# Kernel optimization log

Measured on AMD Instinct MI355X. Metric: run time of the kernel, lower is better.

The kernel has to match this reference:

```python
import jax, jax.numpy as jnp
import numpy as np

N_EL = 16
N_NUC = 4
N_FEATS = 32
CUTOFF = 10.0
ION_POT = 0.5
ALPHA = 1.0
BATCH = 32768
HIDDEN = 64
I_IDX, J_IDX = np.triu_indices(N_EL, 1)  # electron pairs i<j
N_PAIRS = N_EL * N_NUC + N_EL * (N_EL - 1) // 2
D_IN = N_PAIRS * N_FEATS


def ssp(x):
    # shifted softplus: softplus(x) - log(2), so ssp(0) = 0
    return jax.nn.softplus(x) - jnp.log(2.0).astype(x.dtype)


def setup_inputs() -> dict:
    key = jax.random.key(0)
    ks = jax.random.split(key, 9)
    rs = jax.random.normal(ks[0], (BATCH, N_EL, 3), jnp.float32) * 2.0
    coords = jax.random.normal(ks[1], (N_NUC, 3), jnp.float32)
    charges = jnp.arange(1, N_NUC + 1, dtype=jnp.float32)
    W1 = jax.random.normal(ks[2], (D_IN, HIDDEN), jnp.float32) / jnp.sqrt(D_IN)
    b1 = jnp.zeros((HIDDEN,), jnp.float32)
    W2 = jax.random.normal(ks[3], (HIDDEN, HIDDEN), jnp.float32) / jnp.sqrt(HIDDEN)
    b2 = jnp.zeros((HIDDEN,), jnp.float32)
    W3 = jax.random.normal(ks[4], (HIDDEN, 1), jnp.float32) / jnp.sqrt(HIDDEN)
    b3 = jnp.zeros((1,), jnp.float32)
    return {"rs": rs, "coords": coords, "charges": charges,
            "W1": W1, "b1": b1, "W2": W2, "b2": b2, "W3": W3, "b3": b3}


def reference(rs, coords, charges, W1, b1, W2, b2, W3, b3):
    B = rs.shape[0]
    # electron-nucleus distances: [B, n_el, n_nuc]
    diff_nuc = rs[:, :, None, :] - coords[None, None, :, :]
    dists_nuc = jnp.sqrt(jnp.sum(diff_nuc * diff_nuc, axis=-1))
    # electron-electron distances for pairs i<j: [B, n_el*(n_el-1)//2]
    diff_el = rs[:, I_IDX, :] - rs[:, J_IDX, :]
    dists_el = jnp.sqrt(jnp.sum(diff_el * diff_el, axis=-1))
    dists = jnp.concatenate([dists_nuc.reshape(B, -1), dists_el], axis=1)  # [B, N_PAIRS]
    # Gaussian distance basis expansion
    qs = jnp.linspace(0.0, 1.0, N_FEATS, dtype=rs.dtype)
    mus = CUTOFF * qs ** 2
    sigmas = (1.0 + CUTOFF * qs) / 7.0
    xs = jnp.exp(-((dists[..., None] - mus) ** 2) / sigmas ** 2)  # [B, N_PAIRS, N_FEATS]
    xs = xs.reshape(B, -1)
    # small MLP with shifted-softplus activations
    h = ssp(xs @ W1 + b1)
    h = ssp(h @ W2 + b2)
    ys = (h @ W3 + b3)[:, 0]
    # nuclear asymptotic factor
    decay = jnp.sqrt(2.0 * ION_POT)
    terms = (charges[None, None, :] * dists_nuc + decay * ALPHA * dists_nuc ** 2) / (1.0 + ALPHA * dists_nuc)
    asymp = jnp.exp(-jnp.sum(terms, axis=(1, 2)))
    return jnp.exp(ys) * asymp
```

## Files before the change

### kernel.cpp

```cpp
#include <hip/hip_runtime.h>
#include <math.h>

#define N_EL    16
#define N_NUC   4
#define N_FEATS 32
#define N_PAIRS 184
#define HIDDEN  64
#define TB      32
#define BLOCK   256
#define DLD     185
#define H1LD    68
#define TPW     23
#define WS_PART_OFF (1 << 19)

typedef int   intx8    __attribute__((ext_vector_type(8)));
typedef float floatx16 __attribute__((ext_vector_type(16)));

__constant__ unsigned char c_I[120] = {
    0,0,0,0,0,0,0,0,0,0,0,0,0,0,0,
    1,1,1,1,1,1,1,1,1,1,1,1,1,1,
    2,2,2,2,2,2,2,2,2,2,2,2,2,
    3,3,3,3,3,3,3,3,3,3,3,3,
    4,4,4,4,4,4,4,4,4,4,4,
    5,5,5,5,5,5,5,5,5,5,
    6,6,6,6,6,6,6,6,6,
    7,7,7,7,7,7,7,7,
    8,8,8,8,8,8,8,
    9,9,9,9,9,9,
    10,10,10,10,10,
    11,11,11,11,
    12,12,12,
    13,13,
    14
};
__constant__ unsigned char c_J[120] = {
    1,2,3,4,5,6,7,8,9,10,11,12,13,14,15,
    2,3,4,5,6,7,8,9,10,11,12,13,14,15,
    3,4,5,6,7,8,9,10,11,12,13,14,15,
    4,5,6,7,8,9,10,11,12,13,14,15,
    5,6,7,8,9,10,11,12,13,14,15,
    6,7,8,9,10,11,12,13,14,15,
    7,8,9,10,11,12,13,14,15,
    8,9,10,11,12,13,14,15,
    9,10,11,12,13,14,15,
    10,11,12,13,14,15,
    11,12,13,14,15,
    12,13,14,15,
    13,14,15,
    14,15,
    15
};

__device__ __forceinline__ float ssp(float x) {
    float a = fabsf(x);
    return fmaxf(x, 0.0f) + log1pf(__expf(-a)) - 0.69314718056f;
}
__device__ __forceinline__ float redg(float v) {
    v += __shfl_xor(v, 1);
    v += __shfl_xor(v, 2);
    v += __shfl_xor(v, 4);
    return v;
}

__global__ __launch_bounds__(256)
void prep_w1_kernel(const float* __restrict__ W1, intx8* __restrict__ ws)
{
    __shared__ float w[2 * N_FEATS * HIDDEN];
    const int t = blockIdx.x;
    const float* src = W1 + (size_t)(2 * t) * (N_FEATS * HIDDEN);
    for (int k = threadIdx.x; k < 2 * N_FEATS * HIDDEN; k += 256) w[k] = src[k];
    __syncthreads();

    const int tid = threadIdx.x;
    if (tid >= 128) return;
    const int lane = tid & 63;
    const int nh   = tid >> 6;
    const int lh   = lane >> 5;
    const int col  = nh * 32 + (lane & 31);
    const int fb   = lh * 16;
    intx8 frag;
#pragma unroll
    for (int r = 0; r < 8; ++r) {
        const int pair = r >> 2;
        const int fo   = fb + ((r & 3) << 2);
        const float v0 = 64.0f * w[(pair * N_FEATS + fo + 0) * 64 + col];
        const float v1 = 64.0f * w[(pair * N_FEATS + fo + 1) * 64 + col];
        const float v2 = 64.0f * w[(pair * N_FEATS + fo + 2) * 64 + col];
        const float v3 = 64.0f * w[(pair * N_FEATS + fo + 3) * 64 + col];
        int d = __builtin_amdgcn_cvt_pk_fp8_f32(v0, v1, 0, false);
        d     = __builtin_amdgcn_cvt_pk_fp8_f32(v2, v3, d, true);
        frag[r] = d;
    }
    ws[(size_t)(t * 2 + nh) * 64 + lane] = frag;
}

__global__ __launch_bounds__(BLOCK)
void wfnet_gemm(const float* __restrict__ rs,
                const float* __restrict__ coords,
                const intx8* __restrict__ ws,
                float* __restrict__ partials)
{
    __shared__ float lds_rs[TB * N_EL * 3];
    __shared__ float lds_dist[TB * DLD];

    const int tid  = threadIdx.x;
    const int wave = tid >> 6;
    const int lane = tid & 63;
    const int m    = lane & 31;
    const int lh   = lane >> 5;

    {
        const float* rs_blk = rs + (size_t)blockIdx.x * (TB * N_EL * 3);
        for (int k = tid; k < TB * N_EL * 3; k += BLOCK) lds_rs[k] = rs_blk[k];
    }
    __syncthreads();

    {
        const int bl = tid >> 3, g = tid & 7;
        const float* myrs = lds_rs + bl * (N_EL * 3);
        float* dst = lds_dist + bl * DLD;
        for (int i = 0; i < 8; ++i) {
            const int p = g + 8 * i;
            const int e = p >> 2, n = p & 3;
            const float dx = myrs[e * 3 + 0] - coords[n * 3 + 0];
            const float dy = myrs[e * 3 + 1] - coords[n * 3 + 1];
            const float dz = myrs[e * 3 + 2] - coords[n * 3 + 2];
            dst[p] = sqrtf(dx * dx + dy * dy + dz * dz);
        }
        for (int i = 0; i < 15; ++i) {
            const int q  = g + 8 * i;
            const int ei = 3 * (int)c_I[q], ej = 3 * (int)c_J[q];
            const float dx = myrs[ei + 0] - myrs[ej + 0];
            const float dy = myrs[ei + 1] - myrs[ej + 1];
            const float dz = myrs[ei + 2] - myrs[ej + 2];
            dst[64 + q] = sqrtf(dx * dx + dy * dy + dz * dz);
        }
    }
    __syncthreads();

    const int f0 = lh * 16;
#define MKC(P, FF) float P##1, P##0; { \
    const float fq = (float)(FF) * (1.0f / 31.0f); \
    const float mu = 10.0f * fq * fq; \
    const float is = 7.0f / (1.0f + 10.0f * fq); \
    P##1 = is * 3.3972871404442143f; \
    P##0 = -mu * P##1; }
    MKC(F0_,  f0 + 0)  MKC(F1_,  f0 + 1)  MKC(F2_,  f0 + 2)  MKC(F3_,  f0 + 3)
    MKC(F4_,  f0 + 4)  MKC(F5_,  f0 + 5)  MKC(F6_,  f0 + 6)  MKC(F7_,  f0 + 7)
    MKC(F8_,  f0 + 8)  MKC(F9_,  f0 + 9)  MKC(F10_, f0 + 10) MKC(F11_, f0 + 11)
    MKC(F12_, f0 + 12) MKC(F13_, f0 + 13) MKC(F14_, f0 + 14) MKC(F15_, f0 + 15)
#undef MKC

    floatx16 accA = {};
    floatx16 accB = {};
    const intx8* wq = ws + ((size_t)(wave * TPW) * 128 + lane);
    const float* drow = lds_dist + m * DLD + wave * (2 * TPW);

#define XZ(dd, P) ({ const float t_ = fmaf(dd, P##1, P##0); fmaf(t_, -t_, 56.5f); })
#define PKD(dd, A, B, C, D) ({ \
    unsigned w_; \
    w_ = __builtin_amdgcn_cvt_pk_u8_f32(XZ(dd, A), 0, 0u); \
    w_ = __builtin_amdgcn_cvt_pk_u8_f32(XZ(dd, B), 1, w_); \
    w_ = __builtin_amdgcn_cvt_pk_u8_f32(XZ(dd, C), 2, w_); \
    w_ = __builtin_amdgcn_cvt_pk_u8_f32(XZ(dd, D), 3, w_); \
    (int)w_; })
#define MKA8(AV, dx0, dx1) \
    intx8 AV; { \
    AV[0] = PKD(dx0, F0_,  F1_,  F2_,  F3_);  \
    AV[1] = PKD(dx0, F4_,  F5_,  F6_,  F7_);  \
    AV[2] = PKD(dx0, F8_,  F9_,  F10_, F11_); \
    AV[3] = PKD(dx0, F12_, F13_, F14_, F15_); \
    AV[4] = PKD(dx1, F0_,  F1_,  F2_,  F3_);  \
    AV[5] = PKD(dx1, F4_,  F5_,  F6_,  F7_);  \
    AV[6] = PKD(dx1, F8_,  F9_,  F10_, F11_); \
    AV[7] = PKD(dx1, F12_, F13_, F14_, F15_); }
#define KROUND(AV, Q0, Q1) { \
    accA = __builtin_amdgcn_mfma_scale_f32_32x32x64_f8f6f4( \
               AV, Q0, accA, 0, 0, 0, 0x7F7F7F7F, 0, 0x79797979); \
    accB = __builtin_amdgcn_mfma_scale_f32_32x32x64_f8f6f4( \
               AV, Q1, accB, 0, 0, 0, 0x7F7F7F7F, 0, 0x79797979); }

    intx8 pA0 = wq[0],   pA1 = wq[64];
    intx8 pB0 = wq[128], pB1 = wq[192];
    float dA0 = drow[0], dA1 = drow[1];
    float dB0 = drow[2], dB1 = drow[3];

    for (int it = 0; it < 10; ++it) {
        const intx8* wn = wq + 256;
        const float eA0 = drow[4 * it + 4], eA1 = drow[4 * it + 5];
        const float eB0 = drow[4 * it + 6], eB1 = drow[4 * it + 7];

        { MKA8(av, dA0, dA1) KROUND(av, pA0, pA1) }
        pA0 = wn[0]; pA1 = wn[64];

        { MKA8(bv, dB0, dB1) KROUND(bv, pB0, pB1) }
        pB0 = wn[128]; pB1 = wn[192];

        wq = wn;
        dA0 = eA0; dA1 = eA1; dB0 = eB0; dB1 = eB1;
    }
    {
        const intx8* wn = wq + 256;
        const float eA0 = drow[44], eA1 = drow[45];
        { MKA8(av, dA0, dA1) KROUND(av, pA0, pA1) }
        pA0 = wn[0]; pA1 = wn[64];
        { MKA8(bv, dB0, dB1) KROUND(bv, pB0, pB1) }
        { MKA8(cv, eA0, eA1) KROUND(cv, pA0, pA1) }
    }
#undef KROUND
#undef MKA8
#undef PKD
#undef XZ

    float* pdst = partials + ((size_t)blockIdx.x * 4 + wave) * 2048;
#pragma unroll
    for (int rg = 0; rg < 16; ++rg) {
        const int el = (rg & 3) + 8 * (rg >> 2) + 4 * lh;
        pdst[el * 64 + m]      = accA[rg];
        pdst[el * 64 + 32 + m] = accB[rg];
    }
}

__global__ __launch_bounds__(BLOCK)
void wfnet_tail(const float* __restrict__ rs,
                const float* __restrict__ coords,
                const float* __restrict__ charges,
                const float* __restrict__ partials,
                const float* __restrict__ b1,
                const float* __restrict__ W2,
                const float* __restrict__ b2,
                const float* __restrict__ W3,
                const float* __restrict__ b3,
                float* __restrict__ out)
{
    __shared__ float lds_rs[TB * N_EL * 3];
    __shared__ float lds_h1[TB * H1LD];
    __shared__ float lds_w2[HIDDEN * HIDDEN];

    const int tid = threadIdx.x;
    const int el  = tid >> 3;
    const int g   = tid & 7;
    const int b   = blockIdx.x * TB + el;

    {
        const float* rs_blk = rs + (size_t)blockIdx.x * (TB * N_EL * 3);
        for (int k = tid; k < TB * N_EL * 3; k += BLOCK) lds_rs[k] = rs_blk[k];
    }
    {
        float4* dst = (float4*)lds_w2;
        const float4* src = (const float4*)W2;
#pragma unroll
        for (int i = 0; i < 4; ++i) dst[tid + 256 * i] = src[tid + 256 * i];
    }

    {
        const float* pb = partials + (size_t)blockIdx.x * 8192 + el * 64 + g * 8;
        const float4 p00 = ((const float4*)(pb + 0 * 2048))[0];
        const float4 p01 = ((const float4*)(pb + 0 * 2048))[1];
        const float4 p10 = ((const float4*)(pb + 1 * 2048))[0];
        const float4 p11 = ((const float4*)(pb + 1 * 2048))[1];
        const float4 p20 = ((const float4*)(pb + 2 * 2048))[0];
        const float4 p21 = ((const float4*)(pb + 2 * 2048))[1];
        const float4 p30 = ((const float4*)(pb + 3 * 2048))[0];
        const float4 p31 = ((const float4*)(pb + 3 * 2048))[1];
        const float4 ba = ((const float4*)(b1 + g * 8))[0];
        const float4 bb = ((const float4*)(b1 + g * 8))[1];
        float* h1w = lds_h1 + el * H1LD + g * 8;
        h1w[0] = ssp(p00.x + p10.x + p20.x + p30.x + ba.x);
        h1w[1] = ssp(p00.y + p10.y + p20.y + p30.y + ba.y);
        h1w[2] = ssp(p00.z + p10.z + p20.z + p30.z + ba.z);
        h1w[3] = ssp(p00.w + p10.w + p20.w + p30.w + ba.w);
        h1w[4] = ssp(p01.x + p11.x + p21.x + p31.x + bb.x);
        h1w[5] = ssp(p01.y + p11.y + p21.y + p31.y + bb.y);
        h1w[6] = ssp(p01.z + p11.z + p21.z + p31.z + bb.z);
        h1w[7] = ssp(p01.w + p11.w + p21.w + p31.w + bb.w);
    }

    float asy = 0.0f;
    __syncthreads();
    {
        const float* myrs = lds_rs + el * (N_EL * 3);
        const float4 ch = *(const float4*)charges;
#pragma unroll
        for (int i = 0; i < 8; ++i) {
            const int p = g + 8 * i;
            const int e = p >> 2, n = p & 3;
            const float dx = myrs[e * 3 + 0] - coords[n * 3 + 0];
            const float dy = myrs[e * 3 + 1] - coords[n * 3 + 1];
            const float dz = myrs[e * 3 + 2] - coords[n * 3 + 2];
            const float d = sqrtf(dx * dx + dy * dy + dz * dz);
            const float Z = (n < 2) ? ((n == 0) ? ch.x : ch.y)
                                    : ((n == 2) ? ch.z : ch.w);
            asy += (Z * d + d * d) / (1.0f + d);
        }
    }
    asy = redg(asy);

    const float4* __restrict__ W2v = (const float4*)lds_w2;
    const float4* __restrict__ b2v = (const float4*)b2;
    const int wbi = g * 2;
    const float4 b2a = b2v[wbi], b2b = b2v[wbi + 1];
    float s0 = b2a.x, s1 = b2a.y, s2 = b2a.z, s3 = b2a.w;
    float s4 = b2b.x, s5 = b2b.y, s6 = b2b.z, s7 = b2b.w;

    const float* __restrict__ h1row = lds_h1 + el * H1LD;
    for (int k = 0; k < HIDDEN; ++k) {
        const float hk  = h1row[k];
        const float4 wa = W2v[k * 16 + wbi];
        const float4 wb = W2v[k * 16 + wbi + 1];
        s0 = fmaf(hk, wa.x, s0); s1 = fmaf(hk, wa.y, s1);
        s2 = fmaf(hk, wa.z, s2); s3 = fmaf(hk, wa.w, s3);
        s4 = fmaf(hk, wb.x, s4); s5 = fmaf(hk, wb.y, s5);
        s6 = fmaf(hk, wb.z, s6); s7 = fmaf(hk, wb.w, s7);
    }

    const float4* __restrict__ W3v = (const float4*)W3;
    const float4 w3a = W3v[wbi], w3b = W3v[wbi + 1];
    float part = ssp(s0) * w3a.x + ssp(s1) * w3a.y
               + ssp(s2) * w3a.z + ssp(s3) * w3a.w
               + ssp(s4) * w3b.x + ssp(s5) * w3b.y
               + ssp(s6) * w3b.z + ssp(s7) * w3b.w;
    part = redg(part);

    if (g == 0) {
        const float ys = part + b3[0];
        out[b] = __expf(ys) * __expf(-asy);
    }
}

extern "C" void kernel_launch(void* const* d_in, const int* in_sizes, int n_in,
                              void* d_out, int out_size, void* d_ws, size_t ws_size,
                              hipStream_t stream) {
    const float* rs      = (const float*)d_in[0];
    const float* coords  = (const float*)d_in[1];
    const float* charges = (const float*)d_in[2];
    const float* W1      = (const float*)d_in[3];
    const float* b1      = (const float*)d_in[4];
    const float* W2      = (const float*)d_in[5];
    const float* b2      = (const float*)d_in[6];
    const float* W3      = (const float*)d_in[7];
    const float* b3      = (const float*)d_in[8];
    float* out = (float*)d_out;

    const int batch = in_sizes[0] / (N_EL * 3);
    intx8* w1f8     = (intx8*)d_ws;
    float* partials = (float*)((char*)d_ws + WS_PART_OFF);

    prep_w1_kernel<<<N_PAIRS / 2, 256, 0, stream>>>(W1, w1f8);
    wfnet_gemm<<<batch / TB, BLOCK, 0, stream>>>(rs, coords, w1f8, partials);
    wfnet_tail<<<batch / TB, BLOCK, 0, stream>>>(rs, coords, charges, partials,
                                                 b1, W2, b2, W3, b3, out);
}
```

Baseline: 128.7 us.

## Split GEMM K-range across two 128-thread blocks per batch tile

The GEMM kernel now launches twice as many blocks of 128 threads, each handling half of the pair dimension (92 pairs) for a 32-sample tile. Each block computes only its half of the distances into a smaller LDS buffer, and its two waves write partials into the same slots the four waves used to fill. The aim is more blocks, smaller LDS use per block and better occupancy and latency hiding. In exchange, rs is loaded twice per tile and the distance computation gains a per-element branch.

```diff
diff --git a/kernel.cpp b/kernel.cpp
--- a/kernel.cpp
+++ b/kernel.cpp
@@ -7,8 +7,9 @@
 #define N_PAIRS 184
 #define HIDDEN  64
 #define TB      32
-#define BLOCK   256
-#define DLD     185
+#define BLOCK   128
+#define KHALF   92
+#define DLD2    93
 #define H1LD    68
 #define TPW     23
 #define WS_PART_OFF (1 << 19)
@@ -101,39 +102,46 @@
                 float* __restrict__ partials)
 {
     __shared__ float lds_rs[TB * N_EL * 3];
-    __shared__ float lds_dist[TB * DLD];
+    __shared__ float lds_dist[TB * DLD2];
 
     const int tid  = threadIdx.x;
     const int wave = tid >> 6;
     const int lane = tid & 63;
     const int m    = lane & 31;
     const int lh   = lane >> 5;
-
-    {
-        const float* rs_blk = rs + (size_t)blockIdx.x * (TB * N_EL * 3);
+    const int bt   = blockIdx.x >> 1;
+    const int kb   = blockIdx.x & 1;
+    const int g    = kb * 2 + wave;
+
+    {
+        const float* rs_blk = rs + (size_t)bt * (TB * N_EL * 3);
         for (int k = tid; k < TB * N_EL * 3; k += BLOCK) lds_rs[k] = rs_blk[k];
     }
     __syncthreads();
 
     {
-        const int bl = tid >> 3, g = tid & 7;
-        const float* myrs = lds_rs + bl * (N_EL * 3);
-        float* dst = lds_dist + bl * DLD;
-        for (int i = 0; i < 8; ++i) {
-            const int p = g + 8 * i;
-            const int e = p >> 2, n = p & 3;
-            const float dx = myrs[e * 3 + 0] - coords[n * 3 + 0];
-            const float dy = myrs[e * 3 + 1] - coords[n * 3 + 1];
-            const float dz = myrs[e * 3 + 2] - coords[n * 3 + 2];
-            dst[p] = sqrtf(dx * dx + dy * dy + dz * dz);
-        }
-        for (int i = 0; i < 15; ++i) {
-            const int q  = g + 8 * i;
-            const int ei = 3 * (int)c_I[q], ej = 3 * (int)c_J[q];
-            const float dx = myrs[ei + 0] - myrs[ej + 0];
-            const float dy = myrs[ei + 1] - myrs[ej + 1];
-            const float dz = myrs[ei + 2] - myrs[ej + 2];
-            dst[64 + q] = sqrtf(dx * dx + dy * dy + dz * dz);
+        const int row = tid >> 2;
+        const int g4  = tid & 3;
+        const float* myrs = lds_rs + row * (N_EL * 3);
+        float* dst = lds_dist + row * DLD2;
+#pragma unroll
+        for (int i = 0; i < 23; ++i) {
+            const int lp = g4 + 4 * i;
+            const int p  = kb * KHALF + lp;
+            float dx, dy, dz;
+            if (p < 64) {
+                const int e = p >> 2, n = p & 3;
+                dx = myrs[e * 3 + 0] - coords[n * 3 + 0];
+                dy = myrs[e * 3 + 1] - coords[n * 3 + 1];
+                dz = myrs[e * 3 + 2] - coords[n * 3 + 2];
+            } else {
+                const int q  = p - 64;
+                const int ei = 3 * (int)c_I[q], ej = 3 * (int)c_J[q];
+                dx = myrs[ei + 0] - myrs[ej + 0];
+                dy = myrs[ei + 1] - myrs[ej + 1];
+                dz = myrs[ei + 2] - myrs[ej + 2];
+            }
+            dst[lp] = sqrtf(dx * dx + dy * dy + dz * dz);
         }
     }
     __syncthreads();
@@ -153,8 +161,8 @@
 
     floatx16 accA = {};
     floatx16 accB = {};
-    const intx8* wq = ws + ((size_t)(wave * TPW) * 128 + lane);
-    const float* drow = lds_dist + m * DLD + wave * (2 * TPW);
+    const intx8* wq = ws + ((size_t)(g * TPW) * 128 + lane);
+    const float* drow = lds_dist + m * DLD2 + wave * (2 * TPW);
 
 #define XZ(dd, P) ({ const float t_ = fmaf(dd, P##1, P##0); fmaf(t_, -t_, 56.5f); })
 #define PKD(dd, A, B, C, D) ({ \
@@ -212,7 +220,7 @@
 #undef PKD
 #undef XZ
 
-    float* pdst = partials + ((size_t)blockIdx.x * 4 + wave) * 2048;
+    float* pdst = partials + ((size_t)bt * 4 + g) * 2048;
 #pragma unroll
     for (int rg = 0; rg < 16; ++rg) {
         const int el = (rg & 3) + 8 * (rg >> 2) + 4 * lh;
@@ -221,7 +229,7 @@
     }
 }
 
-__global__ __launch_bounds__(BLOCK)
+__global__ __launch_bounds__(256)
 void wfnet_tail(const float* __restrict__ rs,
                 const float* __restrict__ coords,
                 const float* __restrict__ charges,
@@ -244,7 +252,7 @@
 
     {
         const float* rs_blk = rs + (size_t)blockIdx.x * (TB * N_EL * 3);
-        for (int k = tid; k < TB * N_EL * 3; k += BLOCK) lds_rs[k] = rs_blk[k];
+        for (int k = tid; k < TB * N_EL * 3; k += 256) lds_rs[k] = rs_blk[k];
     }
     {
         float4* dst = (float4*)lds_w2;
@@ -347,7 +355,7 @@
     float* partials = (float*)((char*)d_ws + WS_PART_OFF);
 
     prep_w1_kernel<<<N_PAIRS / 2, 256, 0, stream>>>(W1, w1f8);
-    wfnet_gemm<<<batch / TB, BLOCK, 0, stream>>>(rs, coords, w1f8, partials);
-    wfnet_tail<<<batch / TB, BLOCK, 0, stream>>>(rs, coords, charges, partials,
-                                                 b1, W2, b2, W3, b3, out);
-}
+    wfnet_gemm<<<(batch / TB) * 2, BLOCK, 0, stream>>>(rs, coords, w1f8, partials);
+    wfnet_tail<<<batch / TB, 256, 0, stream>>>(rs, coords, charges, partials,
+                                               b1, W2, b2, W3, b3, out);
+}
```

Result: slower. 135.4 us (+5.2%).

## Fuse GEMM and MLP tail kernels via LDS split-K reduction

Applied to the files above, without the earlier changes.

Merges the first-layer FP8 GEMM kernel and the MLP tail kernel into a single kernel. The four waves' split-K partial accumulators are summed in LDS (wave 0 stores, the others use LDS atomicAdd) instead of being written to global memory and read back. The distance buffer's LDS region is reused for the reduction, W2 and h1 through a union. This removes one launch and the global round trip of the partials, at the cost of more LDS per block, extra barriers and serialized LDS atomics.

```diff
diff --git a/kernel.cpp b/kernel.cpp
--- a/kernel.cpp
+++ b/kernel.cpp
@@ -11,7 +11,6 @@
 #define DLD     185
 #define H1LD    68
 #define TPW     23
-#define WS_PART_OFF (1 << 19)
 
 typedef int   intx8    __attribute__((ext_vector_type(8)));
 typedef float floatx16 __attribute__((ext_vector_type(16)));
@@ -95,13 +94,23 @@
 }
 
 __global__ __launch_bounds__(BLOCK)
-void wfnet_gemm(const float* __restrict__ rs,
-                const float* __restrict__ coords,
-                const intx8* __restrict__ ws,
-                float* __restrict__ partials)
+void wfnet_fused(const float* __restrict__ rs,
+                 const float* __restrict__ coords,
+                 const float* __restrict__ charges,
+                 const intx8* __restrict__ ws,
+                 const float* __restrict__ b1,
+                 const float* __restrict__ W2,
+                 const float* __restrict__ b2,
+                 const float* __restrict__ W3,
+                 const float* __restrict__ b3,
+                 float* __restrict__ out)
 {
     __shared__ float lds_rs[TB * N_EL * 3];
-    __shared__ float lds_dist[TB * DLD];
+    __shared__ __align__(16) char lds_u[33280];
+    float* lds_dist = (float*)lds_u;
+    float* red      = (float*)lds_u;
+    float* w2s      = (float*)(lds_u + 8192);
+    float* h1s      = (float*)(lds_u + 24576);
 
     const int tid  = threadIdx.x;
     const int wave = tid >> 6;
@@ -212,78 +221,61 @@
 #undef PKD
 #undef XZ
 
-    float* pdst = partials + ((size_t)blockIdx.x * 4 + wave) * 2048;
-#pragma unroll
-    for (int rg = 0; rg < 16; ++rg) {
-        const int el = (rg & 3) + 8 * (rg >> 2) + 4 * lh;
-        pdst[el * 64 + m]      = accA[rg];
-        pdst[el * 64 + 32 + m] = accB[rg];
-    }
-}
-
-__global__ __launch_bounds__(BLOCK)
-void wfnet_tail(const float* __restrict__ rs,
-                const float* __restrict__ coords,
-                const float* __restrict__ charges,
-                const float* __restrict__ partials,
-                const float* __restrict__ b1,
-                const float* __restrict__ W2,
-                const float* __restrict__ b2,
-                const float* __restrict__ W3,
-                const float* __restrict__ b3,
-                float* __restrict__ out)
-{
-    __shared__ float lds_rs[TB * N_EL * 3];
-    __shared__ float lds_h1[TB * H1LD];
-    __shared__ float lds_w2[HIDDEN * HIDDEN];
-
-    const int tid = threadIdx.x;
-    const int el  = tid >> 3;
-    const int g   = tid & 7;
-    const int b   = blockIdx.x * TB + el;
-
-    {
-        const float* rs_blk = rs + (size_t)blockIdx.x * (TB * N_EL * 3);
-        for (int k = tid; k < TB * N_EL * 3; k += BLOCK) lds_rs[k] = rs_blk[k];
-    }
-    {
-        float4* dst = (float4*)lds_w2;
-        const float4* src = (const float4*)W2;
-#pragma unroll
-        for (int i = 0; i < 4; ++i) dst[tid + 256 * i] = src[tid + 256 * i];
-    }
-
-    {
-        const float* pb = partials + (size_t)blockIdx.x * 8192 + el * 64 + g * 8;
-        const float4 p00 = ((const float4*)(pb + 0 * 2048))[0];
-        const float4 p01 = ((const float4*)(pb + 0 * 2048))[1];
-        const float4 p10 = ((const float4*)(pb + 1 * 2048))[0];
-        const float4 p11 = ((const float4*)(pb + 1 * 2048))[1];
-        const float4 p20 = ((const float4*)(pb + 2 * 2048))[0];
-        const float4 p21 = ((const float4*)(pb + 2 * 2048))[1];
-        const float4 p30 = ((const float4*)(pb + 3 * 2048))[0];
-        const float4 p31 = ((const float4*)(pb + 3 * 2048))[1];
-        const float4 ba = ((const float4*)(b1 + g * 8))[0];
-        const float4 bb = ((const float4*)(b1 + g * 8))[1];
-        float* h1w = lds_h1 + el * H1LD + g * 8;
-        h1w[0] = ssp(p00.x + p10.x + p20.x + p30.x + ba.x);
-        h1w[1] = ssp(p00.y + p10.y + p20.y + p30.y + ba.y);
-        h1w[2] = ssp(p00.z + p10.z + p20.z + p30.z + ba.z);
-        h1w[3] = ssp(p00.w + p10.w + p20.w + p30.w + ba.w);
-        h1w[4] = ssp(p01.x + p11.x + p21.x + p31.x + bb.x);
-        h1w[5] = ssp(p01.y + p11.y + p21.y + p31.y + bb.y);
-        h1w[6] = ssp(p01.z + p11.z + p21.z + p31.z + bb.z);
-        h1w[7] = ssp(p01.w + p11.w + p21.w + p31.w + bb.w);
-    }
-
+    const float4* W2g = (const float4*)W2;
+    const float4 w2r0 = W2g[tid];
+    const float4 w2r1 = W2g[tid + 256];
+    const float4 w2r2 = W2g[tid + 512];
+    const float4 w2r3 = W2g[tid + 768];
+
+    __syncthreads();
+
+    if (wave == 0) {
+#pragma unroll
+        for (int rg = 0; rg < 16; ++rg) {
+            const int el = (rg & 3) + 8 * (rg >> 2) + 4 * lh;
+            red[el * 64 + m]      = accA[rg];
+            red[el * 64 + 32 + m] = accB[rg];
+        }
+    }
+    {
+        float4* w2v = (float4*)w2s;
+        w2v[tid]       = w2r0;
+        w2v[tid + 256] = w2r1;
+        w2v[tid + 512] = w2r2;
+        w2v[tid + 768] = w2r3;
+    }
+    __syncthreads();
+
+    if (wave != 0) {
+#pragma unroll
+        for (int rg = 0; rg < 16; ++rg) {
+            const int el = (rg & 3) + 8 * (rg >> 2) + 4 * lh;
+            atomicAdd(&red[el * 64 + m],      accA[rg]);
+            atomicAdd(&red[el * 64 + 32 + m], accB[rg]);
+        }
+    }
+    __syncthreads();
+
+    {
+        const float b1c = b1[tid & 63];
+#pragma unroll
+        for (int k = 0; k < 8; ++k) {
+            const int idx = tid + 256 * k;
+            const int el  = idx >> 6;
+            const int c   = tid & 63;
+            h1s[el * H1LD + c] = ssp(red[idx] + b1c);
+        }
+    }
+
+    const int el2 = tid >> 3;
+    const int g2  = tid & 7;
     float asy = 0.0f;
-    __syncthreads();
-    {
-        const float* myrs = lds_rs + el * (N_EL * 3);
+    {
+        const float* myrs = lds_rs + el2 * (N_EL * 3);
         const float4 ch = *(const float4*)charges;
 #pragma unroll
         for (int i = 0; i < 8; ++i) {
-            const int p = g + 8 * i;
+            const int p = g2 + 8 * i;
             const int e = p >> 2, n = p & 3;
             const float dx = myrs[e * 3 + 0] - coords[n * 3 + 0];
             const float dy = myrs[e * 3 + 1] - coords[n * 3 + 1];
@@ -295,15 +287,16 @@
         }
     }
     asy = redg(asy);
-
-    const float4* __restrict__ W2v = (const float4*)lds_w2;
+    __syncthreads();
+
+    const float4* __restrict__ W2v = (const float4*)w2s;
     const float4* __restrict__ b2v = (const float4*)b2;
-    const int wbi = g * 2;
+    const int wbi = g2 * 2;
     const float4 b2a = b2v[wbi], b2b = b2v[wbi + 1];
     float s0 = b2a.x, s1 = b2a.y, s2 = b2a.z, s3 = b2a.w;
     float s4 = b2b.x, s5 = b2b.y, s6 = b2b.z, s7 = b2b.w;
 
-    const float* __restrict__ h1row = lds_h1 + el * H1LD;
+    const float* __restrict__ h1row = h1s + el2 * H1LD;
     for (int k = 0; k < HIDDEN; ++k) {
         const float hk  = h1row[k];
         const float4 wa = W2v[k * 16 + wbi];
@@ -322,9 +315,9 @@
                + ssp(s6) * w3b.z + ssp(s7) * w3b.w;
     part = redg(part);
 
-    if (g == 0) {
+    if (g2 == 0) {
         const float ys = part + b3[0];
-        out[b] = __expf(ys) * __expf(-asy);
+        out[blockIdx.x * TB + el2] = __expf(ys) * __expf(-asy);
     }
 }
 
@@ -344,10 +337,8 @@
 
     const int batch = in_sizes[0] / (N_EL * 3);
     intx8* w1f8     = (intx8*)d_ws;
-    float* partials = (float*)((char*)d_ws + WS_PART_OFF);
 
     prep_w1_kernel<<<N_PAIRS / 2, 256, 0, stream>>>(W1, w1f8);
-    wfnet_gemm<<<batch / TB, BLOCK, 0, stream>>>(rs, coords, w1f8, partials);
-    wfnet_tail<<<batch / TB, BLOCK, 0, stream>>>(rs, coords, charges, partials,
-                                                 b1, W2, b2, W3, b3, out);
-}
+    wfnet_fused<<<batch / TB, BLOCK, 0, stream>>>(rs, coords, charges, w1f8,
+                                                  b1, W2, b2, W3, b3, out);
+}
```

Result: slower. 151.7 us (+17.9%).
